# Kernel optimization log

Measured on AMD Instinct MI355X. Metric: run time of the kernel, lower is better.

Reference implementation:

```python
import jax, jax.numpy as jnp
import numpy as np

COMMITMENT_COST = 0.25


def setup_inputs() -> dict:
    key = jax.random.key(0)
    k1, k2 = jax.random.split(key)
    B, D, H, W, K = 32, 64, 64, 64, 1024
    z_e = jax.random.normal(k1, (B, D, H, W), dtype=jnp.float32)
    # codebook initialized uniform(-1/K, 1/K) as in the torch module
    embedding = jax.random.uniform(k2, (K, D), dtype=jnp.float32,
                                   minval=-1.0 / K, maxval=1.0 / K)
    return {"z_e": z_e, "embedding": embedding}


def reference(z_e, embedding):
    B, D, H, W = z_e.shape
    # [B,D,H,W] -> [N, D] with N = B*H*W
    z_flat = jnp.transpose(z_e, (0, 2, 3, 1)).reshape(-1, D)
    # squared L2 distances [N, K] via expansion (same math as torch)
    dists = (jnp.sum(z_flat * z_flat, axis=1, keepdims=True)
             + jnp.sum(embedding * embedding, axis=1)
             - 2.0 * jnp.matmul(z_flat, embedding.T))
    indices_flat = jnp.argmin(dists, axis=1)            # [N]
    z_q_flat = embedding[indices_flat]                  # gather [N, D]
    z_q = jnp.transpose(z_q_flat.reshape(B, H, W, D), (0, 3, 1, 2))
    # straight-through estimator
    z_q_st = z_e + jax.lax.stop_gradient(z_q - z_e)
    vq_loss = jnp.mean((z_q - jax.lax.stop_gradient(z_e)) ** 2)
    commitment_loss = COMMITMENT_COST * jnp.mean((z_e - jax.lax.stop_gradient(z_q)) ** 2)
    indices = indices_flat.reshape(B, H, W)
    return z_q_st, indices, vq_loss, commitment_loss
```

## Files before the change

### kernel.cpp

```cpp
#include <hip/hip_runtime.h>

#define BB 32
#define DD 64
#define HWSZ 4096
#define KK 1024
#define NPIX (BB*HWSZ)
#define NELEM (NPIX*DD)

#define IDX_OUT_OFF NELEM
#define LOSS_OFF (IDX_OUT_OFF + NPIX)

#define WS_E2    0
#define WS_EBH   4096
#define WS_EBL   (WS_EBH + KK*DD*2)
#define WS_IDX   (WS_EBL + KK*DD*2)
#define WS_LIST  (WS_IDX + NPIX*4)
#define WS_CNT   (WS_LIST + NPIX*4)
#define WS_PART  (WS_CNT + 64)
#define WS_ZROWS (WS_PART + 16384)

#define PXB 128
#define ZSTR 129

#define SHIFT 0.25f
#define BAND 2.5e-4f

typedef __attribute__((ext_vector_type(8))) short short8v;
typedef __attribute__((ext_vector_type(4))) float float4v;

__device__ __forceinline__ unsigned short bf16_rne(float f) {
    unsigned u = __float_as_uint(f);
    u += 0x7fffu + ((u >> 16) & 1u);
    return (unsigned short)(u >> 16);
}
__device__ __forceinline__ float bf16_tof(unsigned short h) {
    return __uint_as_float(((unsigned)h) << 16);
}

__device__ __forceinline__ float np_sumsq64(const float* a) {
#pragma clang fp contract(off)
    float r0=0.f,r1=0.f,r2=0.f,r3=0.f,r4=0.f,r5=0.f,r6=0.f,r7=0.f;
#pragma unroll
    for (int i = 0; i < 64; i += 8) {
        r0 += a[i+0]*a[i+0]; r1 += a[i+1]*a[i+1];
        r2 += a[i+2]*a[i+2]; r3 += a[i+3]*a[i+3];
        r4 += a[i+4]*a[i+4]; r5 += a[i+5]*a[i+5];
        r6 += a[i+6]*a[i+6]; r7 += a[i+7]*a[i+7];
    }
    return ((r0+r1)+(r2+r3))+((r4+r5)+(r6+r7));
}

__device__ __forceinline__ float np_sumsq64_lds(const float* sh) {
#pragma clang fp contract(off)
    float r0=0.f,r1=0.f,r2=0.f,r3=0.f,r4=0.f,r5=0.f,r6=0.f,r7=0.f;
#pragma unroll
    for (int i = 0; i < 64; i += 8) {
        float a0=sh[i+0],a1=sh[i+1],a2=sh[i+2],a3=sh[i+3];
        float a4=sh[i+4],a5=sh[i+5],a6=sh[i+6],a7=sh[i+7];
        r0 += a0*a0; r1 += a1*a1; r2 += a2*a2; r3 += a3*a3;
        r4 += a4*a4; r5 += a5*a5; r6 += a6*a6; r7 += a7*a7;
    }
    return ((r0+r1)+(r2+r3))+((r4+r5)+(r6+r7));
}

__device__ __forceinline__ float np_sumsq64_str(const float* sh, int stride) {
#pragma clang fp contract(off)
    float r0=0.f,r1=0.f,r2=0.f,r3=0.f,r4=0.f,r5=0.f,r6=0.f,r7=0.f;
#pragma unroll
    for (int i = 0; i < 64; i += 8) {
        float a0=sh[(i+0)*stride],a1=sh[(i+1)*stride];
        float a2=sh[(i+2)*stride],a3=sh[(i+3)*stride];
        float a4=sh[(i+4)*stride],a5=sh[(i+5)*stride];
        float a6=sh[(i+6)*stride],a7=sh[(i+7)*stride];
        r0 += a0*a0; r1 += a1*a1; r2 += a2*a2; r3 += a3*a3;
        r4 += a4*a4; r5 += a5*a5; r6 += a6*a6; r7 += a7*a7;
    }
    return ((r0+r1)+(r2+r3))+((r4+r5)+(r6+r7));
}

__global__ __launch_bounds__(256) void vq_prep(const float* __restrict__ emb,
                                               short* __restrict__ ebh,
                                               short* __restrict__ ebl,
                                               float* __restrict__ e2) {
    int t    = blockIdx.x * 256 + threadIdx.x;
    int l    = t & 63;
    int slot = t >> 6;
    int ct = slot >> 1, ks = slot & 1;
    int code  = ct*16 + (l & 15);
    int dbase = ks*32 + (l >> 4)*8;
    const float* ep = emb + (size_t)code*DD + dbase;
    short8v h, lo;
#pragma unroll
    for (int j = 0; j < 8; ++j) {
        float v = ep[j];
        unsigned short hh = bf16_rne(v);
        h[j]  = (short)hh;
        lo[j] = (short)bf16_rne(v - bf16_tof(hh));
    }
    ((short8v*)ebh)[t] = h;
    ((short8v*)ebl)[t] = lo;

    if (blockIdx.x < 4) {
        int k = blockIdx.x * 256 + threadIdx.x;
        float ek[DD];
        const float4* p = reinterpret_cast<const float4*>(emb + (size_t)k * DD);
#pragma unroll
        for (int q = 0; q < 16; ++q) {
            float4 v = p[q];
            ek[4*q+0]=v.x; ek[4*q+1]=v.y; ek[4*q+2]=v.z; ek[4*q+3]=v.w;
        }
        e2[k] = np_sumsq64(ek);
    }
}

__global__ __launch_bounds__(256, 4) void vq_main(
        const float* __restrict__ z, const float* __restrict__ emb,
        const short* __restrict__ ebh, const short* __restrict__ ebl,
        const float* __restrict__ e2,
        int* __restrict__ idx, int* __restrict__ list, int* __restrict__ cnt,
        float* __restrict__ zrows, int zcap,
        float* __restrict__ out, double* __restrict__ partial) {
    __shared__ float   zsh[DD * ZSTR];
    __shared__ short8v sb[2][2][128];
    __shared__ float   e2sh[KK];
    __shared__ int     idx_loc[PXB];
    __shared__ int     flpx[128], flslot[128];
    __shared__ int     q_px[128], q_k1[128], q_k2[128];
    __shared__ int     nfl, n2c;
    __shared__ double  sred[256];
    const int tid = threadIdx.x;
    const int w   = tid >> 6;
    const int l   = tid & 63;
    const int lr  = l & 15;
    const int lg  = l >> 4;
    const int b   = blockIdx.x >> 5;
    const int hw0 = (blockIdx.x & 31) * PXB;
    const float* zb = z + (size_t)b*(DD*HWSZ) + hw0;
    const short8v* EBH = (const short8v*)ebh;
    const short8v* EBL = (const short8v*)ebl;
    const int slot = tid & 127, half = tid >> 7;

    if (tid == 0) { nfl = 0; n2c = 0; }
    {
        const int row = tid >> 7, col = tid & 127;
#pragma unroll 8
        for (int d0 = 0; d0 < DD; d0 += 2)
            zsh[(d0+row)*ZSTR + col] = zb[(size_t)(d0+row)*HWSZ + col];
    }
#pragma unroll
    for (int i = 0; i < 4; ++i)
        e2sh[tid + i*256] = e2[tid + i*256] + SHIFT;
    sb[0][half][slot] = (half ? EBL : EBH)[slot];
    __syncthreads();

    short8v ah[2][2], al[2][2];
#pragma unroll
    for (int rt = 0; rt < 2; ++rt) {
#pragma unroll
        for (int ks = 0; ks < 2; ++ks) {
            int px = w*32 + rt*16 + lr;
            int dbase = ks*32 + lg*8;
#pragma unroll
            for (int j = 0; j < 8; ++j) {
                float v = zsh[(dbase + j)*ZSTR + px];
                unsigned short hh = bf16_rne(v);
                ah[rt][ks][j] = (short)hh;
                al[rt][ks][j] = (short)bf16_rne(v - bf16_tof(hh));
            }
        }
    }

    float b1a[2][4], b2a[2][4], b3a[2][4];
#pragma unroll
    for (int rt = 0; rt < 2; ++rt)
#pragma unroll
        for (int r = 0; r < 4; ++r) {
            b1a[rt][r] = 3.4e38f; b2a[rt][r] = 3.4e38f; b3a[rt][r] = 3.4e38f;
        }

    float4v  accP[2];
    float    e2P;
    unsigned kfP;

    {
        short8v bh0 = sb[0][0][l], bh1 = sb[0][0][64+l];
        short8v bl0 = sb[0][1][l], bl1 = sb[0][1][64+l];
        e2P = e2sh[lr];
        kfP = (unsigned)lr;
#pragma unroll
        for (int rt = 0; rt < 2; ++rt) {
            float4v acc = {0.f, 0.f, 0.f, 0.f};
            acc = __builtin_amdgcn_mfma_f32_16x16x32_bf16(ah[rt][0], bh0, acc, 0,0,0);
            acc = __builtin_amdgcn_mfma_f32_16x16x32_bf16(ah[rt][1], bh1, acc, 0,0,0);
            acc = __builtin_amdgcn_mfma_f32_16x16x32_bf16(ah[rt][0], bl0, acc, 0,0,0);
            acc = __builtin_amdgcn_mfma_f32_16x16x32_bf16(ah[rt][1], bl1, acc, 0,0,0);
            acc = __builtin_amdgcn_mfma_f32_16x16x32_bf16(al[rt][0], bh0, acc, 0,0,0);
            acc = __builtin_amdgcn_mfma_f32_16x16x32_bf16(al[rt][1], bh1, acc, 0,0,0);
            accP[rt] = acc;
        }
    }

#pragma unroll 1
    for (int ct = 1; ct < 64; ++ct) {
        const int buf = ct & 1;
        short8v stg = (half ? EBL : EBH)[ct*128 + slot];

#pragma unroll
        for (int rt = 0; rt < 2; ++rt)
#pragma unroll
            for (int r = 0; r < 4; ++r) {
                float s = __builtin_fmaf(-2.f, accP[rt][r], e2P);
                float p = __uint_as_float(
                    (__float_as_uint(s) & ~1023u) | kfP);
                float ob1 = b1a[rt][r], ob2 = b2a[rt][r];
                b1a[rt][r] = fminf(ob1, p);
                b2a[rt][r] = __builtin_amdgcn_fmed3f(ob1, ob2, p);
                b3a[rt][r] = __builtin_amdgcn_fmed3f(ob2, b3a[rt][r], p);
            }

        sb[buf][half][slot] = stg;
        __syncthreads();

        {
            short8v bh0 = sb[buf][0][l], bh1 = sb[buf][0][64+l];
            short8v bl0 = sb[buf][1][l], bl1 = sb[buf][1][64+l];
#pragma unroll
            for (int rt = 0; rt < 2; ++rt) {
                float4v acc = {0.f, 0.f, 0.f, 0.f};
                acc = __builtin_amdgcn_mfma_f32_16x16x32_bf16(ah[rt][0], bh0, acc, 0,0,0);
                acc = __builtin_amdgcn_mfma_f32_16x16x32_bf16(ah[rt][1], bh1, acc, 0,0,0);
                acc = __builtin_amdgcn_mfma_f32_16x16x32_bf16(ah[rt][0], bl0, acc, 0,0,0);
                acc = __builtin_amdgcn_mfma_f32_16x16x32_bf16(ah[rt][1], bl1, acc, 0,0,0);
                acc = __builtin_amdgcn_mfma_f32_16x16x32_bf16(al[rt][0], bh0, acc, 0,0,0);
                acc = __builtin_amdgcn_mfma_f32_16x16x32_bf16(al[rt][1], bh1, acc, 0,0,0);
                accP[rt] = acc;
            }
        }
        e2P = e2sh[ct*16 + lr];
        kfP = (unsigned)(ct*16 + lr);
    }

#pragma unroll
    for (int rt = 0; rt < 2; ++rt)
#pragma unroll
        for (int r = 0; r < 4; ++r) {
            float s = __builtin_fmaf(-2.f, accP[rt][r], e2P);
            float p = __uint_as_float((__float_as_uint(s) & ~1023u) | kfP);
            float ob1 = b1a[rt][r], ob2 = b2a[rt][r];
            b1a[rt][r] = fminf(ob1, p);
            b2a[rt][r] = __builtin_amdgcn_fmed3f(ob1, ob2, p);
            b3a[rt][r] = __builtin_amdgcn_fmed3f(ob2, b3a[rt][r], p);
        }

#pragma unroll
    for (int rt = 0; rt < 2; ++rt) {
#pragma unroll
        for (int r = 0; r < 4; ++r) {
            float b1 = b1a[rt][r], b2 = b2a[rt][r], b3 = b3a[rt][r];
#pragma unroll
            for (int m = 1; m < 16; m <<= 1) {
                float o1 = __shfl_xor(b1, m, 64);
                float o2 = __shfl_xor(b2, m, 64);
                float o3 = __shfl_xor(b3, m, 64);
                float mx  = fmaxf(b1, o1);
                float mn2 = fminf(b2, o2);
                float n1 = fminf(b1, o1);
                float n2 = fminf(mx, mn2);
                float n3 = fminf(fminf(fmaxf(mn2, mx), fmaxf(b2, o2)),
                                 fminf(b3, o3));
                b1 = n1; b2 = n2; b3 = n3;
            }
            if (lr == 0) {
                int i1 = (int)(__float_as_uint(b1) & 1023u);
                int pxl = w*32 + rt*16 + lg*4 + r;
                int n   = b*HWSZ + hw0 + pxl;
                idx[n] = i1;
                idx_loc[pxl] = i1;
                if (b2 - b1 <= BAND) {
                    if (b3 - b1 <= BAND) {
                        int p = atomicAdd(cnt, 1);
                        list[p] = n;
                        int j = atomicAdd(&nfl, 1);
                        flpx[j] = pxl; flslot[j] = p;
                    } else {
                        int i2 = (int)(__float_as_uint(b2) & 1023u);
                        int j = atomicAdd(&n2c, 1);
                        q_px[j] = pxl; q_k1[j] = i1; q_k2[j] = i2;
                    }
                }
            }
        }
    }

    __syncthreads();
    if (tid < n2c) {
        int px = q_px[tid], k1 = q_k1[tid], k2 = q_k2[tid];
        float z2 = np_sumsq64_str(&zsh[px], ZSTR);
        const float* ep1 = emb + (size_t)k1 * DD;
        const float* ep2 = emb + (size_t)k2 * DD;
        float s1 = 0.f, s2 = 0.f;
#pragma unroll
        for (int d = 0; d < DD; ++d) {
            float zd = zsh[d*ZSTR + px];
            s1 = __builtin_fmaf(zd, ep1[d], s1);
            s2 = __builtin_fmaf(zd, ep2[d], s2);
        }
        float B1v, B2v;
        {
#pragma clang fp contract(off)
            float A1 = z2 + e2[k1]; B1v = __builtin_fmaf(-2.f, s1, A1);
            float A2 = z2 + e2[k2]; B2v = __builtin_fmaf(-2.f, s2, A2);
        }
        int win;
        if (k1 < k2) win = (B2v < B1v) ? k2 : k1;
        else         win = (B1v < B2v) ? k1 : k2;
        idx[b*HWSZ + hw0 + px] = win;
        idx_loc[px] = win;
    }

    __syncthreads();
    int nf = nfl;
    for (int j0 = 0; j0 < nf; j0 += 4) {
        int jj = j0 + (tid >> 6);
        if (jj < nf) {
            int sl = flslot[jj];
            if (sl < zcap) {
                int d = tid & 63;
                zrows[(size_t)sl*64 + d] = zsh[d*ZSTR + flpx[jj]];
            }
        }
    }
    __syncthreads();

    {
        const int px = tid & 127;
        const int dh = tid >> 7;
        const int ki = idx_loc[px];
        const float4* ep = reinterpret_cast<const float4*>(
                               emb + (size_t)ki*DD + dh*32);
        float* op = out + (size_t)b*(DD*HWSZ) + (size_t)(dh*32)*HWSZ + hw0 + px;
        float lsum = 0.f;
#pragma unroll
        for (int q = 0; q < 8; ++q) {
            float4 v = ep[q];
            int d = dh*32 + 4*q;
            float z0 = zsh[(d+0)*ZSTR + px];
            float z1 = zsh[(d+1)*ZSTR + px];
            float z2v = zsh[(d+2)*ZSTR + px];
            float z3 = zsh[(d+3)*ZSTR + px];
            op[(size_t)(4*q+0)*HWSZ] = v.x;
            op[(size_t)(4*q+1)*HWSZ] = v.y;
            op[(size_t)(4*q+2)*HWSZ] = v.z;
            op[(size_t)(4*q+3)*HWSZ] = v.w;
            float f0 = v.x - z0, f1 = v.y - z1, f2 = v.z - z2v, f3 = v.w - z3;
            lsum = __builtin_fmaf(f0, f0, lsum);
            lsum = __builtin_fmaf(f1, f1, lsum);
            lsum = __builtin_fmaf(f2, f2, lsum);
            lsum = __builtin_fmaf(f3, f3, lsum);
        }
        if (dh == 0) out[IDX_OUT_OFF + b*HWSZ + hw0 + px] = (float)ki;
        sred[tid] = (double)lsum;
    }
    __syncthreads();
#pragma unroll
    for (int sdown = 128; sdown > 0; sdown >>= 1) {
        if (tid < sdown) sred[tid] += sred[tid + sdown];
        __syncthreads();
    }
    if (tid == 0) partial[blockIdx.x] = sred[0];
}

__global__ __launch_bounds__(256) void vq_exact8(
        const float* __restrict__ z, const float* __restrict__ emb,
        const float* __restrict__ e2, const float* __restrict__ zrows,
        const int* __restrict__ list, const int* __restrict__ cnt,
        int zcap, int* __restrict__ idx, float* __restrict__ out,
        double* __restrict__ delta) {
    __shared__ float zsh[DD];
    __shared__ float rbv[256];
    __shared__ int   rbi[256];
    __shared__ double dred[64];
    const int tid = threadIdx.x;
    const int C   = *cnt;

    for (int i = blockIdx.x; i < C; i += gridDim.x) {
        const int n = list[i];
        if (tid < 64) {
            if (i < zcap) {
                zsh[tid] = zrows[(size_t)i*64 + tid];
            } else {
                zsh[tid] = z[(size_t)(n>>12)*(DD*HWSZ) + (n&4095)
                             + (size_t)tid*HWSZ];
            }
        }
        __syncthreads();

        const float z2 = np_sumsq64_lds(zsh);

        float bestv = 3.4e38f; int bi = 0x7fffffff;
#pragma unroll
        for (int c = 0; c < 4; ++c) {
            int k = c*256 + tid;
            const float4* ep = reinterpret_cast<const float4*>(emb + (size_t)k*DD);
            float s = 0.f;
#pragma unroll
            for (int q = 0; q < 16; ++q) {
                float4 v = ep[q];
                s = __builtin_fmaf(zsh[4*q+0], v.x, s);
                s = __builtin_fmaf(zsh[4*q+1], v.y, s);
                s = __builtin_fmaf(zsh[4*q+2], v.z, s);
                s = __builtin_fmaf(zsh[4*q+3], v.w, s);
            }
            float Bv;
            {
#pragma clang fp contract(off)
                float A = z2 + e2[k];
                Bv = __builtin_fmaf(-2.f, s, A);
            }
            if (Bv < bestv) { bestv = Bv; bi = k; }
        }

        rbv[tid] = bestv; rbi[tid] = bi;
        __syncthreads();
#pragma unroll
        for (int sdown = 128; sdown > 0; sdown >>= 1) {
            if (tid < sdown) {
                float ov = rbv[tid + sdown]; int oi = rbi[tid + sdown];
                if (ov < rbv[tid] || (ov == rbv[tid] && oi < rbi[tid])) {
                    rbv[tid] = ov; rbi[tid] = oi;
                }
            }
            __syncthreads();
        }
        const int win = rbi[0];
        const int old = idx[n];
        if (win != old) {
            const int bq = n >> 12, hw = n & 4095;
            if (tid < 64) {
                float zd = zsh[tid];
                float en = emb[(size_t)win*DD + tid];
                float eo = emb[(size_t)old*DD + tid];
                out[(size_t)bq*(DD*HWSZ) + (size_t)tid*HWSZ + hw] = en;
                float dn = en - zd, dl = eo - zd;
                dred[tid] = (double)(dn*dn) - (double)(dl*dl);
            }
            __syncthreads();
            if (tid == 0) {
                double s = 0.0;
                for (int j = 0; j < 64; ++j) s += dred[j];
                atomicAdd(delta, s);
                idx[n] = win;
                out[IDX_OUT_OFF + n] = (float)win;
            }
        }
        __syncthreads();
    }
}

__global__ __launch_bounds__(256) void vq_finalize(
        const double* __restrict__ part, const double* __restrict__ delta,
        float* __restrict__ out) {
    __shared__ double sred[256];
    int t = threadIdx.x;
    sred[t] = part[t] + part[t + 256] + part[t + 512] + part[t + 768];
    __syncthreads();
#pragma unroll
    for (int sdown = 128; sdown > 0; sdown >>= 1) {
        if (t < sdown) sred[t] += sred[t + sdown];
        __syncthreads();
    }
    if (t == 0) {
        double m = (sred[0] + *delta) / (double)NELEM;
        out[LOSS_OFF]     = (float)m;
        out[LOSS_OFF + 1] = (float)(0.25 * m);
    }
}

extern "C" void kernel_launch(void* const* d_in, const int* in_sizes, int n_in,
                              void* d_out, int out_size, void* d_ws, size_t ws_size,
                              hipStream_t stream) {
    const float* z   = (const float*)d_in[0];
    const float* emb = (const float*)d_in[1];
    float* out = (float*)d_out;
    char*  ws  = (char*)d_ws;

    float*  e2p   = (float*)(ws + WS_E2);
    short*  ebh   = (short*)(ws + WS_EBH);
    short*  ebl   = (short*)(ws + WS_EBL);
    int*    idxp  = (int*)(ws + WS_IDX);
    int*    lst   = (int*)(ws + WS_LIST);
    int*    cntp  = (int*)(ws + WS_CNT);
    double* delta = (double*)(ws + WS_CNT + 8);
    double* part  = (double*)(ws + WS_PART);
    float*  zrows = (float*)(ws + WS_ZROWS);

    long long zrem = (long long)ws_size - (long long)WS_ZROWS;
    int zcap = zrem > 0 ? (int)(zrem / 256) : 0;
    if (zcap > NPIX) zcap = NPIX;

    hipMemsetAsync(cntp, 0, 16, stream);
    vq_prep     <<<32,       256, 0, stream>>>(emb, ebh, ebl, e2p);
    vq_main     <<<NPIX/PXB, 256, 0, stream>>>(z, emb, ebh, ebl, e2p, idxp,
                                               lst, cntp, zrows, zcap,
                                               out, part);
    vq_exact8   <<<512,      256, 0, stream>>>(z, emb, e2p, zrows, lst, cntp,
                                               zcap, idxp, out, delta);
    vq_finalize <<<1,        256, 0, stream>>>(part, delta, out);
}
```

Before: 122.9 us.

## Overlay shared buffers, drop e2 LDS copy, prefetch codebook tile one iteration ahead

Shared-memory arrays used in different phases now share a single 8 KB overlay region, and the 4 KB e2 table in LDS is dropped in favour of direct global reads of e2 each tile. This shrinks LDS per block, which may let more blocks fit per CU. The codebook staging load is issued one iteration earlier (register double-buffering), and the LDS store plus barrier move ahead of the argmin update so that global load latency is better hidden. Extra barriers are added to reinitialise the counters, and the e2 value is now a dependent global load inside the loop.

Measured after the change: 125.0 us. About the same (+1.7%).

```diff
diff --git a/kernel.cpp b/kernel.cpp
--- a/kernel.cpp
+++ b/kernel.cpp
@@ -120,14 +120,18 @@
         int* __restrict__ idx, int* __restrict__ list, int* __restrict__ cnt,
         float* __restrict__ zrows, int zcap,
         float* __restrict__ out, double* __restrict__ partial) {
-    __shared__ float   zsh[DD * ZSTR];
-    __shared__ short8v sb[2][2][128];
-    __shared__ float   e2sh[KK];
-    __shared__ int     idx_loc[PXB];
-    __shared__ int     flpx[128], flslot[128];
-    __shared__ int     q_px[128], q_k1[128], q_k2[128];
-    __shared__ int     nfl, n2c;
-    __shared__ double  sred[256];
+    __shared__ float zsh[DD * ZSTR];
+    __shared__ __align__(16) char ovl[8192];
+    short8v* sbp    = (short8v*)ovl;
+    int*     idx_loc= (int*)ovl;
+    int*     flpx   = (int*)(ovl + 512);
+    int*     flslot = (int*)(ovl + 1024);
+    int*     q_px   = (int*)(ovl + 1536);
+    int*     q_k1   = (int*)(ovl + 2048);
+    int*     q_k2   = (int*)(ovl + 2560);
+    int*     cnts   = (int*)(ovl + 3072);
+    double*  sred   = (double*)(ovl + 4096);
+
     const int tid = threadIdx.x;
     const int w   = tid >> 6;
     const int l   = tid & 63;
@@ -139,18 +143,15 @@
     const short8v* EBH = (const short8v*)ebh;
     const short8v* EBL = (const short8v*)ebl;
     const int slot = tid & 127, half = tid >> 7;
-
-    if (tid == 0) { nfl = 0; n2c = 0; }
+    const short8v* EBX = half ? EBL : EBH;
+
     {
         const int row = tid >> 7, col = tid & 127;
 #pragma unroll 8
         for (int d0 = 0; d0 < DD; d0 += 2)
             zsh[(d0+row)*ZSTR + col] = zb[(size_t)(d0+row)*HWSZ + col];
     }
-#pragma unroll
-    for (int i = 0; i < 4; ++i)
-        e2sh[tid + i*256] = e2[tid + i*256] + SHIFT;
-    sb[0][half][slot] = (half ? EBL : EBH)[slot];
+    sbp[half*128 + slot] = EBX[slot];
     __syncthreads();
 
     short8v ah[2][2], al[2][2];
@@ -181,11 +182,13 @@
     float4v  accP[2];
     float    e2P;
     unsigned kfP;
+    short8v  stgC;
 
     {
-        short8v bh0 = sb[0][0][l], bh1 = sb[0][0][64+l];
-        short8v bl0 = sb[0][1][l], bl1 = sb[0][1][64+l];
-        e2P = e2sh[lr];
+        stgC = EBX[128 + slot];
+        short8v bh0 = sbp[l],       bh1 = sbp[64+l];
+        short8v bl0 = sbp[128+l],   bl1 = sbp[192+l];
+        e2P = e2[lr] + SHIFT;
         kfP = (unsigned)lr;
 #pragma unroll
         for (int rt = 0; rt < 2; ++rt) {
@@ -202,8 +205,10 @@
 
 #pragma unroll 1
     for (int ct = 1; ct < 64; ++ct) {
-        const int buf = ct & 1;
-        short8v stg = (half ? EBL : EBH)[ct*128 + slot];
+        const int base = (ct & 1) * 256;
+        short8v stgN = EBX[((ct+1) & 63)*128 + slot];
+        sbp[base + half*128 + slot] = stgC;
+        __syncthreads();
 
 #pragma unroll
         for (int rt = 0; rt < 2; ++rt)
@@ -218,12 +223,9 @@
                 b3a[rt][r] = __builtin_amdgcn_fmed3f(ob2, b3a[rt][r], p);
             }
 
-        sb[buf][half][slot] = stg;
-        __syncthreads();
-
         {
-            short8v bh0 = sb[buf][0][l], bh1 = sb[buf][0][64+l];
-            short8v bl0 = sb[buf][1][l], bl1 = sb[buf][1][64+l];
+            short8v bh0 = sbp[base + l],     bh1 = sbp[base + 64+l];
+            short8v bl0 = sbp[base + 128+l], bl1 = sbp[base + 192+l];
 #pragma unroll
             for (int rt = 0; rt < 2; ++rt) {
                 float4v acc = {0.f, 0.f, 0.f, 0.f};
@@ -236,8 +238,9 @@
                 accP[rt] = acc;
             }
         }
-        e2P = e2sh[ct*16 + lr];
+        e2P = e2[ct*16 + lr] + SHIFT;
         kfP = (unsigned)(ct*16 + lr);
+        stgC = stgN;
     }
 
 #pragma unroll
@@ -251,6 +254,12 @@
             b2a[rt][r] = __builtin_amdgcn_fmed3f(ob1, ob2, p);
             b3a[rt][r] = __builtin_amdgcn_fmed3f(ob2, b3a[rt][r], p);
         }
+
+    __syncthreads();
+    if (tid < 2) cnts[tid] = 0;
+    __syncthreads();
+    int& nfl = cnts[0];
+    int& n2c = cnts[1];
 
 #pragma unroll
     for (int rt = 0; rt < 2; ++rt) {
```
